# Kernel tuning notes

Hardware: AMD Instinct MI355X
Metric: run time of the kernel (lower is better)

The kernel has to match this reference:

```python
import jax, jax.numpy as jnp
import numpy as np

N, E, K_ORDER = 50000, 800000, 3
F_IN, H = 128, 128


def setup_inputs() -> dict:
    key = jax.random.key(0)
    ks = jax.random.split(key, 24)
    s = 0.05
    inp = {
        "x_t": jax.random.normal(ks[0], (N, F_IN), jnp.float32),
        "h_prev": jax.random.normal(ks[1], (N, H), jnp.float32),
        "c_prev": jax.random.normal(ks[2], (N, H), jnp.float32),
        "edge_weight": jax.random.uniform(ks[3], (E,), jnp.float32),
        "edge_index": jax.random.randint(ks[4], (2, E), 0, N, dtype=jnp.int64),
    }
    # Input->gate weight matrices W_* : (F, H)
    for i, nm in enumerate(["W_i", "W_f", "W_c", "W_o"]):
        inp[nm] = jax.random.normal(ks[5 + i], (F_IN, H), jnp.float32) * s
    # ChebConv weights theta_* : (K, H, H) applied to hidden state
    for i, nm in enumerate(["theta_i", "theta_f", "theta_c", "theta_o"]):
        inp[nm] = jax.random.normal(ks[9 + i], (K_ORDER, H, H), jnp.float32) * s
    # Gate biases (b_* of GCLSTM merged with the ChebConv bias; they add)
    for i, nm in enumerate(["b_i", "b_f", "b_c", "b_o"]):
        inp[nm] = jax.random.normal(ks[13 + i], (H,), jnp.float32) * s
    # Peephole weights w_c_* : (H,)
    for i, nm in enumerate(["w_ci", "w_cf", "w_co"]):
        inp[nm] = jax.random.normal(ks[17 + i], (H,), jnp.float32) * s
    return inp


def _cheb_norm(edge_index, edge_weight):
    # get_laplacian('sym') + lambda_max=2 scaling + add_self_loops(-1)
    # => L~ = -D^{-1/2} A D^{-1/2}  (zero diagonal)
    src, dst = edge_index[0], edge_index[1]
    deg = jax.ops.segment_sum(edge_weight, src, num_segments=N)
    dinv = jnp.where(deg > 0, jax.lax.rsqrt(jnp.maximum(deg, 1e-30)), 0.0)
    return src, dst, -edge_weight * dinv[src] * dinv[dst]


def _cheb_conv(x, theta, bias, src, dst, wn):
    # Chebyshev recursion: Tx0=x, Tx1=L~x, Tx_k = 2 L~ Tx_{k-1} - Tx_{k-2}
    def Lmul(v):
        return jax.ops.segment_sum(wn[:, None] * v[src], dst, num_segments=N)
    Tx0 = x
    Tx1 = Lmul(x)
    out = Tx0 @ theta[0] + Tx1 @ theta[1]
    for k in range(2, theta.shape[0]):
        Tx2 = 2.0 * Lmul(Tx1) - Tx0
        out = out + Tx2 @ theta[k]
        Tx0, Tx1 = Tx1, Tx2
    return out + bias


def reference(x_t, h_prev, c_prev, edge_weight, W_i, W_f, W_c, W_o,
              theta_i, theta_f, theta_c, theta_o, b_i, b_f, b_c, b_o,
              w_ci, w_cf, w_co, edge_index):
    src, dst, wn = _cheb_norm(edge_index, edge_weight)
    i = jax.nn.sigmoid(x_t @ W_i + _cheb_conv(h_prev, theta_i, b_i, src, dst, wn)
                       + w_ci * c_prev)
    f = jax.nn.sigmoid(x_t @ W_f + _cheb_conv(h_prev, theta_f, b_f, src, dst, wn)
                       + w_cf * c_prev)
    t = jnp.tanh(x_t @ W_c + _cheb_conv(h_prev, theta_c, b_c, src, dst, wn))
    c_t = f * c_prev + i * t
    o = jax.nn.sigmoid(x_t @ W_o + _cheb_conv(h_prev, theta_o, b_o, src, dst, wn)
                       + w_co * c_t)
    h_t = o * jnp.tanh(c_t)
    return (h_t, c_t)
```

## Files before the change

### kernel.cpp

```cpp
#include <hip/hip_runtime.h>

#define NN 50000
#define EE 800000
#define KC 64
#define EPC (EE / KC)
#define DEG_SCALE 4096.0f

typedef float f32x4 __attribute__((ext_vector_type(4)));
typedef short bf16x8 __attribute__((ext_vector_type(8)));
typedef unsigned short u16x8 __attribute__((ext_vector_type(8)));

__device__ __forceinline__ unsigned short f2bf(float f) {
  unsigned int u = __float_as_uint(f);
  u += 0x7fffu + ((u >> 16) & 1u);
  return (unsigned short)(u >> 16);
}
__device__ __forceinline__ float bf2f(unsigned short u) {
  return __uint_as_float(((unsigned int)u) << 16);
}

__device__ __forceinline__ void async_copy16(const void* g, void* l) {
  __builtin_amdgcn_global_load_lds(
      (const __attribute__((address_space(1))) unsigned int*)g,
      (__attribute__((address_space(3))) unsigned int*)l, 16, 0, 0);
}

__device__ __forceinline__ unsigned short* hslot2(char* o, long j) {
  return (unsigned short*)(o + (j >> 7) * 512 + (j & 127) * 2);
}
__device__ __forceinline__ void store8u16(char* o, long s, uint4 v) {
  *(uint4*)(o + (s >> 7) * 512 + (s & 127) * 2) = v;
}
#define CNT_SLOT0 3200000L
#define RANK_SLOT0 3200000L

__global__ __launch_bounds__(1024) void k_pre(
    const float* __restrict__ Wi, const float* __restrict__ Wf,
    const float* __restrict__ Wc, const float* __restrict__ Wo,
    const float* __restrict__ Ti, const float* __restrict__ Tf,
    const float* __restrict__ Tc, const float* __restrict__ To,
    unsigned short* __restrict__ bglob, const float* __restrict__ h,
    const float* __restrict__ x, char* __restrict__ outB,
    const int* __restrict__ src, const int* __restrict__ dst,
    const float* __restrict__ w) {
  __shared__ unsigned hist[25000];
  const int b = blockIdx.x, tid = threadIdx.x;
  char* cB = outB + (long)NN * 512;
  if (b < KC) {
    uint4* h4 = (uint4*)hist;
    const int base = b * EPC;
    for (int j = tid; j < 6250; j += 1024) h4[j] = (uint4){0u, 0u, 0u, 0u};
    __syncthreads();
    for (int k = tid; k < EPC; k += 1024) {
      const int e = base + k;
      const int d = dst[e];
      const int sh = (d & 1) * 16;
      const unsigned old = atomicAdd(&hist[d >> 1], 1u << sh);
      *hslot2(cB, RANK_SLOT0 + e) = (unsigned short)((old >> sh) & 0xffffu);
    }
    __syncthreads();
    for (int j = tid; j < 6250; j += 1024)
      store8u16(outB, CNT_SLOT0 + (long)b * NN + j * 8, h4[j]);
    __syncthreads();
    for (int j = tid; j < 6250; j += 1024) h4[j] = (uint4){0u, 0u, 0u, 0u};
    __syncthreads();
    for (int k = tid; k < EPC; k += 1024) {
      const int e = base + k;
      const int s = src[e];
      const unsigned q = (unsigned)__float2uint_rn(w[e] * DEG_SCALE);
      const int sh = (s & 1) * 16;
      atomicAdd(&hist[s >> 1], q << sh);
    }
    __syncthreads();
    for (int j = tid; j < 6250; j += 1024)
      store8u16(outB, (long)b * NN + j * 8, h4[j]);
  } else if (b < KC + 32) {
    const int t = (b - KC) * 1024 + tid;
    const int ks = t >> 11;
    const int cf = (t >> 6) & 31;
    const int lane = t & 63;
    const int wv = cf >> 3, hl = (cf >> 2) & 1, g = cf & 3;
    const int kg = lane >> 4, lm = lane & 15;
    const int hc = (wv * 2 + hl) * 16 + lm;
    const float* Wg = (g == 0) ? Wi : (g == 1) ? Wf : (g == 2) ? Wc : Wo;
    const float* Tg = (g == 0) ? Ti : (g == 1) ? Tf : (g == 2) ? Tc : To;
    u16x8 out;
#pragma unroll
    for (int dk = 0; dk < 8; ++dk) {
      const int k = ks * 32 + kg * 8 + dk;
      const int kb = k >> 7, r = k & 127;
      const float v = (kb == 0) ? Wg[r * 128 + hc] : Tg[(kb - 1) * 16384 + r * 128 + hc];
      out[dk] = f2bf(v);
    }
    *(u16x8*)(bglob + t * 8) = out;
  } else if (b < KC + 32 + 782) {
    const int i = (b - (KC + 32)) * 1024 + tid;
    if (i < 100000 * 8) {
      const float* hp = h + i * 8;
      const f32x4 v0 = *(const f32x4*)hp;
      const f32x4 v1 = *(const f32x4*)(hp + 4);
      u16x8 o;
#pragma unroll
      for (int e = 0; e < 4; ++e) o[e] = f2bf(v0[e]);
#pragma unroll
      for (int e = 0; e < 4; ++e) o[e + 4] = f2bf(v1[e]);
      *(u16x8*)(outB + (i >> 4) * 512 + 256 + (i & 15) * 16) = o;
    }
  } else {
    const int i = (b - (KC + 32 + 782)) * 1024 + tid;
    if (i < 100000 * 8) {
      const float* xp = x + i * 8;
      const f32x4 v0 = *(const f32x4*)xp;
      const f32x4 v1 = *(const f32x4*)(xp + 4);
      u16x8 o;
#pragma unroll
      for (int e = 0; e < 4; ++e) o[e] = f2bf(v0[e]);
#pragma unroll
      for (int e = 0; e < 4; ++e) o[e + 4] = f2bf(v1[e]);
      *(u16x8*)(cB + (i >> 4) * 512 + 256 + (i & 15) * 16) = o;
    }
  }
}

__device__ __forceinline__ int block_scan_excl_256(int v, int* total) {
  __shared__ int wsum[4];
  const int tid = threadIdx.x;
  const int lane = tid & 63, wv = tid >> 6;
  int x = v;
#pragma unroll
  for (int d = 1; d < 64; d <<= 1) {
    const int y = __shfl_up(x, d, 64);
    if (lane >= d) x += y;
  }
  if (lane == 63) wsum[wv] = x;
  __syncthreads();
  int pre = 0, tot = 0;
#pragma unroll
  for (int u = 0; u < 4; ++u) {
    const int s = wsum[u];
    pre += (u < wv) ? s : 0;
    tot += s;
  }
  *total = tot;
  return pre + x - v;
}

__global__ void k_phase2(char* __restrict__ outB, float* __restrict__ dinv,
                         int* __restrict__ wscnt, int* __restrict__ bsum) {
  char* cB = outB + (long)NN * 512;
  const int i = blockIdx.x * 256 + threadIdx.x;
  int run = 0;
  if (i < NN) {
    float s = 0.f;
#pragma unroll
    for (int c = 0; c < KC; ++c)
      s += (float)*hslot2(outB, (long)c * NN + i);
    s *= (1.0f / DEG_SCALE);
    dinv[i] = (s > 0.f) ? rsqrtf(fmaxf(s, 1e-30f)) : 0.f;
#pragma unroll
    for (int c = 0; c < KC; ++c) {
      *hslot2(cB, (long)c * NN + i) = (unsigned short)run;
      run += (int)*hslot2(outB, CNT_SLOT0 + (long)c * NN + i);
    }
    wscnt[i] = run;
  }
  int tot;
  block_scan_excl_256(run, &tot);
  if (threadIdx.x == 0) bsum[blockIdx.x] = tot;
}

__global__ void k_scan2(const int* __restrict__ bsum, int* __restrict__ boff,
                        const int nb) {
  const int t = threadIdx.x;
  const int v = (t < nb) ? bsum[t] : 0;
  int tot;
  const int excl = block_scan_excl_256(v, &tot);
  if (t <= nb) boff[t] = excl;
}

__global__ void k_scan3(const int* __restrict__ cnt, const int* __restrict__ boff,
                        int* __restrict__ off) {
  const int i = blockIdx.x * 256 + threadIdx.x;
  const int v = (i < NN) ? cnt[i] : 0;
  int tot;
  const int excl = block_scan_excl_256(v, &tot) + boff[blockIdx.x];
  if (i < NN) off[i] = excl;
  if (i == NN) off[NN] = excl;
}

__global__ void k_edge2(const int* __restrict__ src, const int* __restrict__ dst,
                        const float* __restrict__ w, const float* __restrict__ dinv,
                        const int* __restrict__ off, char* __restrict__ outB,
                        int2* __restrict__ ed) {
  const int e = blockIdx.x * blockDim.x + threadIdx.x;
  if (e >= EE) return;
  char* cB = outB + (long)NN * 512;
  const int s = src[e], d = dst[e];
  const int c = e / EPC;
  const int p = off[d] + (int)*hslot2(cB, (long)c * NN + d) +
                (int)*hslot2(cB, RANK_SLOT0 + e);
  int2 rec;
  rec.x = s;
  rec.y = __float_as_int(-w[e] * dinv[s] * dinv[d]);
  ed[p] = rec;
}

__global__ __launch_bounds__(256) void k_gather(
    const char* __restrict__ vinB, const char* __restrict__ vsubB, const float alpha,
    const int* __restrict__ off, const int2* __restrict__ ed, char* __restrict__ voutB) {
  const int wid = threadIdx.x >> 6, lane = threadIdx.x & 63;
  const int node = blockIdx.x * 4 + wid;
  const int p0 = off[node], p1 = off[node + 1];
  const int lb = lane * 4;
  float ax0 = 0.f, ay0 = 0.f, ax1 = 0.f, ay1 = 0.f;
  float ax2 = 0.f, ay2 = 0.f, ax3 = 0.f, ay3 = 0.f;
  int p = p0;
  for (; p + 7 < p1; p += 8) {
    int2 E[8];
    unsigned V[8];
#pragma unroll
    for (int u = 0; u < 8; ++u) E[u] = ed[p + u];
#pragma unroll
    for (int u = 0; u < 8; ++u)
      V[u] = *(const unsigned*)(vinB + (long)E[u].x * 512 + lb);
#pragma unroll
    for (int u = 0; u < 8; ++u) {
      const float wv = __int_as_float(E[u].y);
      float* ax = (u & 3) == 0 ? &ax0 : (u & 3) == 1 ? &ax1 : (u & 3) == 2 ? &ax2 : &ax3;
      float* ay = (u & 3) == 0 ? &ay0 : (u & 3) == 1 ? &ay1 : (u & 3) == 2 ? &ay2 : &ay3;
      *ax = fmaf(wv, bf2f((unsigned short)V[u]), *ax);
      *ay = fmaf(wv, bf2f((unsigned short)(V[u] >> 16)), *ay);
    }
  }
  for (; p + 3 < p1; p += 4) {
    const int2 e0 = ed[p], e1 = ed[p + 1], e2 = ed[p + 2], e3 = ed[p + 3];
    const unsigned v0 = *(const unsigned*)(vinB + (long)e0.x * 512 + lb);
    const unsigned v1 = *(const unsigned*)(vinB + (long)e1.x * 512 + lb);
    const unsigned v2 = *(const unsigned*)(vinB + (long)e2.x * 512 + lb);
    const unsigned v3 = *(const unsigned*)(vinB + (long)e3.x * 512 + lb);
    const float w0 = __int_as_float(e0.y), w1 = __int_as_float(e1.y);
    const float w2 = __int_as_float(e2.y), w3 = __int_as_float(e3.y);
    ax0 = fmaf(w0, bf2f((unsigned short)v0), ax0);
    ay0 = fmaf(w0, bf2f((unsigned short)(v0 >> 16)), ay0);
    ax1 = fmaf(w1, bf2f((unsigned short)v1), ax1);
    ay1 = fmaf(w1, bf2f((unsigned short)(v1 >> 16)), ay1);
    ax2 = fmaf(w2, bf2f((unsigned short)v2), ax2);
    ay2 = fmaf(w2, bf2f((unsigned short)(v2 >> 16)), ay2);
    ax3 = fmaf(w3, bf2f((unsigned short)v3), ax3);
    ay3 = fmaf(w3, bf2f((unsigned short)(v3 >> 16)), ay3);
  }
  for (; p < p1; ++p) {
    const int2 e0 = ed[p];
    const unsigned v0 = *(const unsigned*)(vinB + (long)e0.x * 512 + lb);
    const float w0 = __int_as_float(e0.y);
    ax0 = fmaf(w0, bf2f((unsigned short)v0), ax0);
    ay0 = fmaf(w0, bf2f((unsigned short)(v0 >> 16)), ay0);
  }
  float rx = alpha * ((ax0 + ax1) + (ax2 + ax3));
  float ry = alpha * ((ay0 + ay1) + (ay2 + ay3));
  if (vsubB) {
    const unsigned s = *(const unsigned*)(vsubB + (long)node * 512 + lb);
    rx -= bf2f((unsigned short)s);
    ry -= bf2f((unsigned short)(s >> 16));
  }
  const unsigned ow = (unsigned)f2bf(rx) | ((unsigned)f2bf(ry) << 16);
  *(unsigned*)(voutB + (long)node * 512 + lb) = ow;
}

__global__ __launch_bounds__(256, 2) void k_gemm(
    const char* __restrict__ outB, const unsigned short* __restrict__ bglob,
    const float* __restrict__ c_prev,
    const float* __restrict__ b_i, const float* __restrict__ b_f,
    const float* __restrict__ b_c, const float* __restrict__ b_o,
    const float* __restrict__ w_ci, const float* __restrict__ w_cf,
    const float* __restrict__ w_co, float* __restrict__ h_out,
    float* __restrict__ c_out) {
  __shared__ char lds[65536];
  const int tid = threadIdx.x;
  const int lane = tid & 63;
  const int wid = tid >> 6;
  const int kg = lane >> 4;
  const int lm = lane & 15;
  const int m0 = blockIdx.x * 64;

  const char* hB = outB;
  const char* cB = outB + (long)NN * 512;

  const int srow0 = m0 + wid * 16 + lm;
  const long srow = (srow0 < NN) ? srow0 : (NN - 1);
  const int schunk = kg * 16;

#pragma unroll
  for (int ks = 0; ks < 16; ++ks) {
    const char* base = (ks < 4) ? (cB + 256) : (ks < 8) ? (hB + 256) : (ks < 12) ? hB : cB;
    async_copy16(base + srow * 512 + (ks & 3) * 64 + schunk,
                 &lds[ks * 4096 + tid * 16]);
  }

  f32x4 acc[32];
#pragma unroll
  for (int i = 0; i < 32; ++i) acc[i] = (f32x4){0.f, 0.f, 0.f, 0.f};

  bf16x8 b0[8], b1[8];
  auto loadB = [&](int ks, bf16x8* bb) {
    const unsigned short* fp = bglob + ((ks * 32 + wid * 8) * 64 + lane) * 8;
#pragma unroll
    for (int i = 0; i < 8; ++i) bb[i] = *(const bf16x8*)(fp + i * 512);
  };

  __syncthreads();

  loadB(0, b0);
#pragma unroll
  for (int ks = 0; ks < 16; ++ks) {
    bf16x8* bc = (ks & 1) ? b1 : b0;
    bf16x8* bn = (ks & 1) ? b0 : b1;
    if (ks < 15) loadB(ks + 1, bn);
    bf16x8 a[4];
#pragma unroll
    for (int rf = 0; rf < 4; ++rf)
      a[rf] = *(const bf16x8*)(&lds[ks * 4096 + rf * 1024 + lane * 16]);
#pragma unroll
    for (int rf = 0; rf < 4; ++rf)
#pragma unroll
      for (int i = 0; i < 8; ++i)
        acc[rf * 8 + i] =
            __builtin_amdgcn_mfma_f32_16x16x32_bf16(a[rf], bc[i], acc[rf * 8 + i], 0, 0, 0);
  }

#pragma unroll
  for (int hl = 0; hl < 2; ++hl) {
    const int hc = (wid * 2 + hl) * 16 + lm;
    const float bi = b_i[hc], bfv = b_f[hc], bc = b_c[hc], bo = b_o[hc];
    const float wci = w_ci[hc], wcf = w_cf[hc], wco = w_co[hc];
#pragma unroll
    for (int rf = 0; rf < 4; ++rf) {
#pragma unroll
      for (int reg = 0; reg < 4; ++reg) {
        const int node = m0 + rf * 16 + kg * 4 + reg;
        if (node < NN) {
          const float cp = c_prev[node * 128 + hc];
          const float pi = acc[rf * 8 + hl * 4 + 0][reg] + bi + wci * cp;
          const float pf = acc[rf * 8 + hl * 4 + 1][reg] + bfv + wcf * cp;
          const float pc = acc[rf * 8 + hl * 4 + 2][reg] + bc;
          const float po = acc[rf * 8 + hl * 4 + 3][reg] + bo;
          const float ig = 1.f / (1.f + __expf(-pi));
          const float fg = 1.f / (1.f + __expf(-pf));
          const float ct = fg * cp + ig * tanhf(pc);
          const float og = 1.f / (1.f + __expf(-(po + wco * ct)));
          h_out[node * 128 + hc] = og * tanhf(ct);
          c_out[node * 128 + hc] = ct;
        }
      }
    }
  }
}


extern "C" void kernel_launch(void* const* d_in, const int* in_sizes, int n_in,
                              void* d_out, int out_size, void* d_ws, size_t ws_size,
                              hipStream_t stream) {
  const float* x_t    = (const float*)d_in[0];
  const float* h_prev = (const float*)d_in[1];
  const float* c_prev = (const float*)d_in[2];
  const float* ew     = (const float*)d_in[3];
  const int*   eidx   = (const int*)d_in[4];
  const float* Wi = (const float*)d_in[5];
  const float* Wf = (const float*)d_in[6];
  const float* Wc = (const float*)d_in[7];
  const float* Wo = (const float*)d_in[8];
  const float* Ti = (const float*)d_in[9];
  const float* Tf = (const float*)d_in[10];
  const float* Tc = (const float*)d_in[11];
  const float* To = (const float*)d_in[12];
  const float* bi = (const float*)d_in[13];
  const float* bf = (const float*)d_in[14];
  const float* bc = (const float*)d_in[15];
  const float* bo = (const float*)d_in[16];
  const float* wci = (const float*)d_in[17];
  const float* wcf = (const float*)d_in[18];
  const float* wco = (const float*)d_in[19];

  char* ws = (char*)d_ws;
  float* dinv  = (float*)(ws + 0);
  int*   wscnt = (int*)(ws + 200192);
  int*   off   = (int*)(ws + 400384);
  int*   bsum  = (int*)(ws + 601088);
  int*   boff  = (int*)(ws + 602112);
  int2*  ed    = (int2*)(ws + 603136);
  unsigned short* bglob = (unsigned short*)(ws + 7003136);

  char* outB = (char*)d_out;
  float* h_out = (float*)d_out;
  float* c_out = h_out + (long)NN * 128;

  const int* esrc = eidx;
  const int* edst = eidx + EE;

  k_pre<<<KC + 32 + 782 + 782, 1024, 0, stream>>>(
      Wi, Wf, Wc, Wo, Ti, Tf, Tc, To, bglob, h_prev, x_t, outB, esrc, edst, ew);
  k_phase2<<<196, 256, 0, stream>>>(outB, dinv, wscnt, bsum);
  k_scan2<<<1, 256, 0, stream>>>(bsum, boff, 196);
  k_scan3<<<196, 256, 0, stream>>>(wscnt, boff, off);
  k_edge2<<<3125, 256, 0, stream>>>(esrc, edst, ew, dinv, off, outB, ed);
  k_gather<<<12500, 256, 0, stream>>>(outB + 256, nullptr, 1.f, off, ed, outB);
  k_gather<<<12500, 256, 0, stream>>>(outB, outB + 256, 2.f, off, ed,
                                      outB + (long)NN * 512);
  k_gemm<<<782, 256, 0, stream>>>(outB, bglob, c_prev,
                                  bi, bf, bc, bo, wci, wcf, wco, h_out, c_out);
}
```

Baseline: 225.8 us.

## Split gemm across 8 waves per block and use fast sigmoid/tanh

The final gemm+LSTM kernel goes from 4 to 8 waves per 64-row block. Each wave now owns 16 output columns (4 gates × 16) instead of 32, which halves accumulator and B-fragment registers and lets more waves stay resident to hide latency. The LDS staging copy is split across all 512 threads. Sigmoid and tanh now use hardware reciprocal plus exp approximations in place of division and tanhf, which costs some precision and may overflow for large inputs.

```diff
diff --git a/kernel.cpp b/kernel.cpp
--- a/kernel.cpp
+++ b/kernel.cpp
@@ -23,6 +23,13 @@
   __builtin_amdgcn_global_load_lds(
       (const __attribute__((address_space(1))) unsigned int*)g,
       (__attribute__((address_space(3))) unsigned int*)l, 16, 0, 0);
+}
+
+__device__ __forceinline__ float fast_sig(float x) {
+  return __builtin_amdgcn_rcpf(1.f + __expf(-x));
+}
+__device__ __forceinline__ float fast_tanh(float x) {
+  return 1.f - 2.f * __builtin_amdgcn_rcpf(__expf(2.f * x) + 1.f);
 }
 
 __device__ __forceinline__ unsigned short* hslot2(char* o, long j) {
@@ -267,7 +274,7 @@
   *(unsigned*)(voutB + (long)node * 512 + lb) = ow;
 }
 
-__global__ __launch_bounds__(256, 2) void k_gemm(
+__global__ __launch_bounds__(512, 4) void k_gemm(
     const char* __restrict__ outB, const unsigned short* __restrict__ bglob,
     const float* __restrict__ c_prev,
     const float* __restrict__ b_i, const float* __restrict__ b_f,
@@ -278,7 +285,7 @@
   __shared__ char lds[65536];
   const int tid = threadIdx.x;
   const int lane = tid & 63;
-  const int wid = tid >> 6;
+  const int w = tid >> 6;
   const int kg = lane >> 4;
   const int lm = lane & 15;
   const int m0 = blockIdx.x * 64;
@@ -286,26 +293,30 @@
   const char* hB = outB;
   const char* cB = outB + (long)NN * 512;
 
-  const int srow0 = m0 + wid * 16 + lm;
-  const long srow = (srow0 < NN) ? srow0 : (NN - 1);
-  const int schunk = kg * 16;
-
-#pragma unroll
-  for (int ks = 0; ks < 16; ++ks) {
-    const char* base = (ks < 4) ? (cB + 256) : (ks < 8) ? (hB + 256) : (ks < 12) ? hB : cB;
-    async_copy16(base + srow * 512 + (ks & 3) * 64 + schunk,
-                 &lds[ks * 4096 + tid * 16]);
-  }
-
-  f32x4 acc[32];
-#pragma unroll
-  for (int i = 0; i < 32; ++i) acc[i] = (f32x4){0.f, 0.f, 0.f, 0.f};
-
-  bf16x8 b0[8], b1[8];
+  {
+    const int t8 = tid & 255;
+    const int rf = t8 >> 6, ln = t8 & 63;
+    const int srow0 = m0 + rf * 16 + (ln & 15);
+    const long srow = (srow0 < NN) ? srow0 : (NN - 1);
+    const int schunk = (ln >> 4) * 16;
+#pragma unroll
+    for (int i = 0; i < 8; ++i) {
+      const int ks = i * 2 + (tid >> 8);
+      const char* base = (ks < 4) ? (cB + 256) : (ks < 8) ? (hB + 256) : (ks < 12) ? hB : cB;
+      async_copy16(base + srow * 512 + (ks & 3) * 64 + schunk,
+                   &lds[ks * 4096 + t8 * 16]);
+    }
+  }
+
+  f32x4 acc[16];
+#pragma unroll
+  for (int i = 0; i < 16; ++i) acc[i] = (f32x4){0.f, 0.f, 0.f, 0.f};
+
+  bf16x8 b0[4], b1[4];
   auto loadB = [&](int ks, bf16x8* bb) {
-    const unsigned short* fp = bglob + ((ks * 32 + wid * 8) * 64 + lane) * 8;
-#pragma unroll
-    for (int i = 0; i < 8; ++i) bb[i] = *(const bf16x8*)(fp + i * 512);
+    const unsigned short* fp = bglob + ((ks * 32 + w * 4) * 64 + lane) * 8;
+#pragma unroll
+    for (int g = 0; g < 4; ++g) bb[g] = *(const bf16x8*)(fp + g * 512);
   };
 
   __syncthreads();
@@ -323,34 +334,31 @@
 #pragma unroll
     for (int rf = 0; rf < 4; ++rf)
 #pragma unroll
-      for (int i = 0; i < 8; ++i)
-        acc[rf * 8 + i] =
-            __builtin_amdgcn_mfma_f32_16x16x32_bf16(a[rf], bc[i], acc[rf * 8 + i], 0, 0, 0);
-  }
-
-#pragma unroll
-  for (int hl = 0; hl < 2; ++hl) {
-    const int hc = (wid * 2 + hl) * 16 + lm;
-    const float bi = b_i[hc], bfv = b_f[hc], bc = b_c[hc], bo = b_o[hc];
-    const float wci = w_ci[hc], wcf = w_cf[hc], wco = w_co[hc];
-#pragma unroll
-    for (int rf = 0; rf < 4; ++rf) {
-#pragma unroll
-      for (int reg = 0; reg < 4; ++reg) {
-        const int node = m0 + rf * 16 + kg * 4 + reg;
-        if (node < NN) {
-          const float cp = c_prev[node * 128 + hc];
-          const float pi = acc[rf * 8 + hl * 4 + 0][reg] + bi + wci * cp;
-          const float pf = acc[rf * 8 + hl * 4 + 1][reg] + bfv + wcf * cp;
-          const float pc = acc[rf * 8 + hl * 4 + 2][reg] + bc;
-          const float po = acc[rf * 8 + hl * 4 + 3][reg] + bo;
-          const float ig = 1.f / (1.f + __expf(-pi));
-          const float fg = 1.f / (1.f + __expf(-pf));
-          const float ct = fg * cp + ig * tanhf(pc);
-          const float og = 1.f / (1.f + __expf(-(po + wco * ct)));
-          h_out[node * 128 + hc] = og * tanhf(ct);
-          c_out[node * 128 + hc] = ct;
-        }
+      for (int g = 0; g < 4; ++g)
+        acc[rf * 4 + g] =
+            __builtin_amdgcn_mfma_f32_16x16x32_bf16(a[rf], bc[g], acc[rf * 4 + g], 0, 0, 0);
+  }
+
+  const int hc = w * 16 + lm;
+  const float bi = b_i[hc], bfv = b_f[hc], bc_ = b_c[hc], bo = b_o[hc];
+  const float wci = w_ci[hc], wcf = w_cf[hc], wco = w_co[hc];
+#pragma unroll
+  for (int rf = 0; rf < 4; ++rf) {
+#pragma unroll
+    for (int reg = 0; reg < 4; ++reg) {
+      const int node = m0 + rf * 16 + kg * 4 + reg;
+      if (node < NN) {
+        const float cp = c_prev[node * 128 + hc];
+        const float pi = acc[rf * 4 + 0][reg] + bi + wci * cp;
+        const float pf = acc[rf * 4 + 1][reg] + bfv + wcf * cp;
+        const float pc = acc[rf * 4 + 2][reg] + bc_;
+        const float po = acc[rf * 4 + 3][reg] + bo;
+        const float ig = fast_sig(pi);
+        const float fg = fast_sig(pf);
+        const float ct = fg * cp + ig * fast_tanh(pc);
+        const float og = fast_sig(po + wco * ct);
+        h_out[node * 128 + hc] = og * fast_tanh(ct);
+        c_out[node * 128 + hc] = ct;
       }
     }
   }
@@ -406,6 +414,6 @@
   k_gather<<<12500, 256, 0, stream>>>(outB + 256, nullptr, 1.f, off, ed, outB);
   k_gather<<<12500, 256, 0, stream>>>(outB, outB + 256, 2.f, off, ed,
                                       outB + (long)NN * 512);
-  k_gemm<<<782, 256, 0, stream>>>(outB, bglob, c_prev,
+  k_gemm<<<782, 512, 0, stream>>>(outB, bglob, c_prev,
                                   bi, bf, bc, bo, wci, wcf, wco, h_out, c_out);
 }
```

Result: faster. 210.3 us (-6.9%).
